# Performance work log

Measured on AMD Instinct MI355X. Metric: run time of the kernel, lower is better.

## Reference

```python
import jax, jax.numpy as jnp
import numpy as np

B, IN, OUT, E, K = 8192, 512, 720, 16, 2
MOE_TEMP = 1.0


def setup_inputs() -> dict:
    key = jax.random.key(0)
    ks = jax.random.split(key, 5)
    s_in = 1.0 / np.sqrt(IN)
    return {
        "x": jax.random.normal(ks[0], (B, IN), dtype=jnp.float32),
        "Wg": jax.random.normal(ks[1], (IN, E), dtype=jnp.float32) * s_in,
        "bg": jax.random.normal(ks[2], (E,), dtype=jnp.float32) * 0.01,
        "We": jax.random.normal(ks[3], (E, IN, OUT), dtype=jnp.float32) * s_in,
        "be": jax.random.normal(ks[4], (E, OUT), dtype=jnp.float32) * 0.01,
    }


def reference(x, Wg, bg, We, be):
    # Gating (eval mode: no noise, divide by temperature)
    gate = (x @ Wg + bg) / MOE_TEMP                      # [B, E]
    topk_vals, topk_idx = jax.lax.top_k(gate, K)          # [B, K]
    gates = jax.nn.softmax(topk_vals, axis=1)             # [B, K]

    # Dense all-expert forward (as the original module computes)
    expert_out = jnp.einsum('bi,eio->beo', x, We) + be    # [B, E, OUT]
    sel = jnp.take_along_axis(expert_out, topk_idx[:, :, None], axis=1)  # [B, K, OUT]
    output = jnp.sum(gates[:, :, None] * sel, axis=1)     # [B, OUT]

    # Load-balancing loss
    probs = jax.nn.softmax(gate, axis=1)                  # [B, E]
    assign = jnp.argmax(gate, axis=1)                     # [B]
    D = jnp.zeros((E,), dtype=gate.dtype).at[assign].add(1.0) / x.shape[0]
    P = jnp.mean(probs, axis=0)
    lb_loss = jnp.sum(D * P) * E
    return output, lb_loss
```

## Files before the change

kernel.cpp:

```cpp
#include <hip/hip_runtime.h>
#include <hip/hip_bf16.h>


#define BATCH 8192
#define IND   512
#define OUTD  720
#define NEXP  16
#define NGBLK 512

typedef __attribute__((ext_vector_type(8))) short short8;
typedef __attribute__((ext_vector_type(4))) float floatx4;

__device__ __forceinline__ unsigned short f2bf(float f) {
    union { float f; unsigned u; } v; v.f = f;
    unsigned r = v.u + 0x7FFFu + ((v.u >> 16) & 1u);
    return (unsigned short)(r >> 16);
}
__device__ __forceinline__ float bf2f(unsigned short u) {
    union { unsigned u; float f; } v; v.u = ((unsigned)u) << 16;
    return v.f;
}

__device__ __forceinline__ void gl2lds16(const void* g, void* l) {
    __builtin_amdgcn_global_load_lds(
        (const __attribute__((address_space(1))) void*)g,
        (__attribute__((address_space(3))) void*)l, 16, 0, 0);
}

__global__ __launch_bounds__(256) void prep_kernel(
    const float* __restrict__ x, const float* __restrict__ Wg,
    const float* __restrict__ bg, const float* __restrict__ We,
    float* __restrict__ gates, int* __restrict__ rowinfo,
    unsigned char* __restrict__ cnt8, float* __restrict__ Pblk, float* __restrict__ Dblk,
    unsigned short* __restrict__ xb, unsigned short* __restrict__ Wt)
{
    __shared__ __align__(16) char smem[35328];
    int tid = threadIdx.x;

    if (blockIdx.x < NGBLK) {
        float* sWg   = (float*)smem;
        float* sg    = sWg + 16 * 516;
        float* smax  = sg + 16 * 17;
        float* sinv  = smax + 16;
        int*   sasgn = (int*)(sinv + 16);

        int rbase = blockIdx.x * 16;

        const float4* gw4 = (const float4*)Wg;
        #pragma unroll
        for (int j = 0; j < 8; ++j) {
            int f = tid + j * 256;
            float4 v = gw4[f];
            int i  = f >> 2;
            int e0 = (f & 3) * 4;
            sWg[(e0 + 0) * 516 + i] = v.x;
            sWg[(e0 + 1) * 516 + i] = v.y;
            sWg[(e0 + 2) * 516 + i] = v.z;
            sWg[(e0 + 3) * 516 + i] = v.w;
        }

        const float4* gx4 = (const float4*)(x + (size_t)rbase * IND);
        #pragma unroll
        for (int j = 0; j < 4; ++j) {
            int f = tid + j * 256;
            float4 v0 = gx4[2 * f];
            float4 v1 = gx4[2 * f + 1];
            short8 o;
            o[0] = (short)f2bf(v0.x); o[1] = (short)f2bf(v0.y);
            o[2] = (short)f2bf(v0.z); o[3] = (short)f2bf(v0.w);
            o[4] = (short)f2bf(v1.x); o[5] = (short)f2bf(v1.y);
            o[6] = (short)f2bf(v1.z); o[7] = (short)f2bf(v1.w);
            *(short8*)&xb[(size_t)rbase * IND + (size_t)f * 8] = o;
        }
        __syncthreads();

        int r = tid >> 4, e = tid & 15;
        const float4* xr = (const float4*)(x + (size_t)(rbase + r) * IND);
        const float4* wr = (const float4*)&sWg[e * 516];
        float acc = bg[e];
        #pragma unroll 8
        for (int i4 = 0; i4 < 128; ++i4) {
            float4 a = xr[i4], w = wr[i4];
            acc += a.x * w.x + a.y * w.y + a.z * w.z + a.w * w.w;
        }
        sg[r * 17 + e] = acc;
        __syncthreads();

        if (tid < 16) {
            int row = rbase + tid;
            float v0 = -1e30f, v1 = -1e30f; int i0 = 0, i1 = 0;
            float g[16];
            #pragma unroll
            for (int ee = 0; ee < 16; ++ee) {
                float v = sg[tid * 17 + ee]; g[ee] = v;
                if (v > v0)      { v1 = v0; i1 = i0; v0 = v; i0 = ee; }
                else if (v > v1) { v1 = v;  i1 = ee; }
            }
            float e1   = expf(v1 - v0);
            float inv2 = 1.f / (1.f + e1);
            gates[row * 2 + 0] = inv2;
            gates[row * 2 + 1] = e1 * inv2;

            float ssum = 0.f;
            #pragma unroll
            for (int ee = 0; ee < 16; ++ee) ssum += expf(g[ee] - v0);
            smax[tid]  = v0;
            sinv[tid]  = 1.f / ssum;
            sasgn[tid] = i0 | (i1 << 8);
        }
        __syncthreads();

        if (tid < 16) {
            int me  = sasgn[tid];
            int i0  = me & 255, i1 = me >> 8;
            int p0 = 0, p1 = 0;
            for (int rp = 0; rp < tid; ++rp) {
                int a = sasgn[rp];
                int a0 = a & 255, a1 = a >> 8;
                p0 += (a0 == i0) + (a1 == i0);
                p1 += (a0 == i1) + (a1 == i1);
            }
            rowinfo[rbase + tid] = i0 | (i1 << 4) | (p0 << 8) | (p1 << 13);

            int ee = tid;
            int cnt = 0; float D = 0.f, P = 0.f;
            #pragma unroll
            for (int rp = 0; rp < 16; ++rp) {
                int a = sasgn[rp];
                int a0 = a & 255, a1 = a >> 8;
                cnt += (a0 == ee) + (a1 == ee);
                D   += (a0 == ee) ? 1.f : 0.f;
                P   += expf(sg[rp * 17 + ee] - smax[rp]) * sinv[rp];
            }
            cnt8[blockIdx.x * 16 + ee] = (unsigned char)cnt;
            Dblk[blockIdx.x * 16 + ee] = D;
            Pblk[blockIdx.x * 16 + ee] = P;
        }
    } else {
        float* tile = (float*)smem;
        int t  = blockIdx.x - NGBLK;
        int e  = t / 184;
        int rem = t - e * 184;
        int kb = (rem / 23) * 64;
        int ob = (rem % 23) * 32;
        const float* src = We + (size_t)e * (IND * OUTD);

        #pragma unroll
        for (int p = 0; p < 2; ++p) {
            int f  = tid + p * 256;
            int kk = f >> 3;
            int o4 = f & 7;
            float4 v = make_float4(0.f, 0.f, 0.f, 0.f);
            if (ob + o4 * 4 < OUTD)
                v = *(const float4*)&src[(size_t)(kb + kk) * OUTD + ob + o4 * 4];
            tile[(o4 * 4 + 0) * 69 + kk] = v.x;
            tile[(o4 * 4 + 1) * 69 + kk] = v.y;
            tile[(o4 * 4 + 2) * 69 + kk] = v.z;
            tile[(o4 * 4 + 3) * 69 + kk] = v.w;
        }
        __syncthreads();

        int o  = tid >> 3;
        int k8 = tid & 7;
        if (ob + o < OUTD) {
            const float* sp = &tile[o * 69 + k8 * 8];
            short8 wv;
            #pragma unroll
            for (int q = 0; q < 8; ++q) wv[q] = (short)f2bf(sp[q]);
            *(short8*)&Wt[(size_t)e * (OUTD * IND) + (size_t)(ob + o) * IND + kb + k8 * 8] = wv;
        }
    }
}

__global__ __launch_bounds__(256, 4) void moe_mfma_kernel(
    const unsigned short* __restrict__ xb, const unsigned short* __restrict__ Wt,
    const float* __restrict__ be,
    const unsigned char* __restrict__ cnt8, const int* __restrict__ rowinfo,
    const float* __restrict__ gates,
    unsigned short* __restrict__ partial)
{
    int e = blockIdx.z;
    int r0 = blockIdx.y * 128;
    int n0 = blockIdx.x * 96;

    __shared__ unsigned short sAB[14336];
    __shared__ unsigned short sbase[513];
    __shared__ int   schunk[16];
    __shared__ int   srow[128];
    __shared__ float sgw[128];
    __shared__ unsigned short sent[128];

    int tid = threadIdx.x;

    sbase[tid]       = cnt8[tid * 16 + e];
    sbase[tid + 256] = cnt8[(tid + 256) * 16 + e];
    __syncthreads();
    if (tid < 16) {
        int s = 0;
        #pragma unroll
        for (int j = 0; j < 32; ++j) s += sbase[tid * 32 + j];
        schunk[tid] = s;
    }
    __syncthreads();
    if (tid == 0) {
        int run = 0;
        #pragma unroll
        for (int c = 0; c < 16; ++c) { int s = schunk[c]; schunk[c] = run; run += s; }
        sbase[512] = (unsigned short)run;
    }
    __syncthreads();
    if (tid < 16) {
        int run = schunk[tid];
        #pragma unroll
        for (int j = 0; j < 32; ++j) {
            int c = sbase[tid * 32 + j];
            sbase[tid * 32 + j] = (unsigned short)run;
            run += c;
        }
    }
    __syncthreads();
    int n = sbase[512];
    if (r0 >= n) return;

    if (tid < 128) {
        int idx = r0 + tid;
        if (idx < n) {
            int g = 0;
            #pragma unroll
            for (int step = 256; step; step >>= 1)
                if (g + step <= 511 && (int)sbase[g + step] <= idx) g += step;
            int local = idx - (int)sbase[g];
            int row = 0, k = 0;
            #pragma unroll
            for (int r = 0; r < 16; ++r) {
                int info = rowinfo[g * 16 + r];
                int i0 = info & 15, i1 = (info >> 4) & 15;
                int p0 = (info >> 8) & 31, p1 = (info >> 13) & 31;
                if (i0 == e && p0 == local) { row = g * 16 + r; k = 0; }
                if (i1 == e && p1 == local) { row = g * 16 + r; k = 1; }
            }
            srow[tid] = row;
            sgw[tid]  = gates[row * 2 + k];
            sent[tid] = (unsigned short)((row << 1) | k);
        } else { srow[tid] = 0; sgw[tid] = 0.f; sent[tid] = 0; }
    }
    __syncthreads();

    int lane = tid & 63, wave = tid >> 6;
    int lsub = lane >> 3;
    int swz  = (lane & 7) ^ lsub;

    const unsigned short* aglb[4];
    unsigned short* alds[4];
    #pragma unroll
    for (int g = 0; g < 4; ++g) {
        int row = wave * 32 + g * 8 + lsub;
        aglb[g] = xb + (size_t)srow[row] * IND + swz * 8;
        alds[g] = &sAB[(wave * 32 + g * 8) * 64];
    }
    const unsigned short* bglb[3];
    unsigned short* blds[3];
    #pragma unroll
    for (int g = 0; g < 3; ++g) {
        int col = n0 + wave * 24 + g * 8 + lsub;
        if (col >= OUTD) col = 0;
        bglb[g] = Wt + ((size_t)e * OUTD + col) * IND + swz * 8;
        blds[g] = &sAB[8192 + (wave * 24 + g * 8) * 64];
    }

    int l15 = lane & 15, quad = lane >> 4;
    int wm = (wave & 1) * 64, wn = (wave >> 1) * 48;
    int axor = (l15 & 7) * 8;

    floatx4 acc[4][3] = {};

    for (int kt = 0; kt < IND / 64; ++kt) {
        __syncthreads();
        #pragma unroll
        for (int g = 0; g < 4; ++g) gl2lds16(aglb[g] + kt * 64, alds[g]);
        #pragma unroll
        for (int g = 0; g < 3; ++g) gl2lds16(bglb[g] + kt * 64, blds[g]);
        __syncthreads();

        #pragma unroll
        for (int ks = 0; ks < 2; ++ks) {
            int ko = ((ks * 4 + quad) * 8) ^ axor;
            short8 a[4], b[3];
            #pragma unroll
            for (int i = 0; i < 4; ++i) a[i] = *(const short8*)&sAB[(wm + i * 16 + l15) * 64 + ko];
            #pragma unroll
            for (int j = 0; j < 3; ++j) b[j] = *(const short8*)&sAB[8192 + (wn + j * 16 + l15) * 64 + ko];
            #pragma unroll
            for (int i = 0; i < 4; ++i)
                #pragma unroll
                for (int j = 0; j < 3; ++j)
                    acc[i][j] = __builtin_amdgcn_mfma_f32_16x16x32_bf16(a[i], b[j], acc[i][j], 0, 0, 0);
        }
    }

    __syncthreads();
    #pragma unroll
    for (int j = 0; j < 3; ++j) {
        int coll = wn + j * 16 + l15;
        int gcol = n0 + coll;
        float bev = (gcol < OUTD) ? be[e * OUTD + gcol] : 0.f;
        #pragma unroll
        for (int i = 0; i < 4; ++i) {
            #pragma unroll
            for (int rr = 0; rr < 4; ++rr) {
                int rowl = wm + i * 16 + quad * 4 + rr;
                sAB[rowl * 104 + coll] = f2bf(sgw[rowl] * (acc[i][j][rr] + bev));
            }
        }
    }
    __syncthreads();

    #pragma unroll
    for (int p = 0; p < 6; ++p) {
        int c    = tid + p * 256;
        int rowl = c / 12;
        int ch   = c - rowl * 12;
        int gcol = n0 + ch * 8;
        if (gcol < OUTD && r0 + rowl < n) {
            *(short8*)&partial[(size_t)sent[rowl] * OUTD + gcol] =
                *(const short8*)&sAB[rowl * 104 + ch * 8];
        }
    }
}

__global__ __launch_bounds__(256) void combine_kernel(
    const unsigned short* __restrict__ partial,
    const float* __restrict__ Pblk, const float* __restrict__ Dblk,
    float* __restrict__ out)
{
    __shared__ float sredP[256], sredD[256];
    unsigned f = blockIdx.x * 256 + threadIdx.x;
    unsigned b = f / 180u;
    unsigned o4 = (f - b * 180u) * 4u;
    const unsigned short* p0 = partial + (size_t)(2u * b) * OUTD + o4;
    ushort4 u0 = *(const ushort4*)p0;
    ushort4 u1 = *(const ushort4*)(p0 + OUTD);
    float4 rv;
    rv.x = bf2f(u0.x) + bf2f(u1.x);
    rv.y = bf2f(u0.y) + bf2f(u1.y);
    rv.z = bf2f(u0.z) + bf2f(u1.z);
    rv.w = bf2f(u0.w) + bf2f(u1.w);
    *(float4*)(out + (size_t)b * OUTD + o4) = rv;

    if (blockIdx.x == 0) {
        int tid = threadIdx.x;
        int e = tid & 15, stripe = tid >> 4;
        float accP = 0.f, accD = 0.f;
        for (int j = 0; j < 32; ++j) {
            int g = stripe * 32 + j;
            accP += Pblk[g * 16 + e];
            accD += Dblk[g * 16 + e];
        }
        sredP[tid] = accP; sredD[tid] = accD;
        __syncthreads();
        if (tid == 0) {
            float s = 0.f;
            for (int ee = 0; ee < 16; ++ee) {
                float P = 0.f, D = 0.f;
                #pragma unroll
                for (int st = 0; st < 16; ++st) { P += sredP[st * 16 + ee]; D += sredD[st * 16 + ee]; }
                s += (D / (float)BATCH) * (P / (float)BATCH);
            }
            out[(size_t)BATCH * OUTD] = s * (float)NEXP;
        }
    }
}

extern "C" void kernel_launch(void* const* d_in, const int* in_sizes, int n_in,
                              void* d_out, int out_size, void* d_ws, size_t ws_size,
                              hipStream_t stream)
{
    const float* x  = (const float*)d_in[0];
    const float* Wg = (const float*)d_in[1];
    const float* bg = (const float*)d_in[2];
    const float* We = (const float*)d_in[3];
    const float* be = (const float*)d_in[4];
    float* out = (float*)d_out;

    char* ws = (char*)d_ws;
    float* gates   = (float*)ws;
    int*   rowinfo = (int*)(ws + 65536);
    unsigned char* cnt8 = (unsigned char*)(ws + 98304);
    float* Pblk    = (float*)(ws + 106496);
    float* Dblk    = (float*)(ws + 139264);
    size_t off_xb  = 172032;
    unsigned short* xb = (unsigned short*)(ws + off_xb);
    size_t off_wt = off_xb + (size_t)BATCH * IND * 2;
    unsigned short* Wt = (unsigned short*)(ws + off_wt);
    size_t off_pt = off_wt + (size_t)NEXP * OUTD * IND * 2;
    unsigned short* partial = (unsigned short*)(ws + off_pt);

    prep_kernel<<<NGBLK + 2944, 256, 0, stream>>>(x, Wg, bg, We, gates, rowinfo,
                                                  cnt8, Pblk, Dblk, xb, Wt);

    dim3 grid(8, 10, NEXP);
    moe_mfma_kernel<<<grid, 256, 0, stream>>>(xb, Wt, be, cnt8, rowinfo, gates, partial);

    combine_kernel<<<(BATCH * (OUTD / 4)) / 256, 256, 0, stream>>>(partial, Pblk, Dblk, out);
}
```

Measured before the change: 140.7 us.

## Drop LDS staging of gate weights and double transpose tile depth in prep kernel

The gating blocks no longer stage Wg into shared memory. Each thread now reads Wg straight from global memory, where it is cached because every block reads the same data. This shrinks the shared-memory allocation, removes a barrier, and allows a launch bound of 8 blocks per CU. The weight-transpose blocks now handle 128 k-rows per tile instead of 64, halving the transpose block count and giving each thread two bf16 vector stores. The trade-off is strided, uncoalesced scalar global loads of Wg in the gating dot product, plus larger per-block transpose work.

```diff
diff --git a/kernel.cpp b/kernel.cpp
--- a/kernel.cpp
+++ b/kernel.cpp
@@ -27,37 +27,23 @@
         (__attribute__((address_space(3))) void*)l, 16, 0, 0);
 }
 
-__global__ __launch_bounds__(256) void prep_kernel(
+__global__ __launch_bounds__(256, 8) void prep_kernel(
     const float* __restrict__ x, const float* __restrict__ Wg,
     const float* __restrict__ bg, const float* __restrict__ We,
     float* __restrict__ gates, int* __restrict__ rowinfo,
     unsigned char* __restrict__ cnt8, float* __restrict__ Pblk, float* __restrict__ Dblk,
     unsigned short* __restrict__ xb, unsigned short* __restrict__ Wt)
 {
-    __shared__ __align__(16) char smem[35328];
+    __shared__ __align__(16) char smem[16896];
     int tid = threadIdx.x;
 
     if (blockIdx.x < NGBLK) {
-        float* sWg   = (float*)smem;
-        float* sg    = sWg + 16 * 516;
+        float* sg    = (float*)smem;
         float* smax  = sg + 16 * 17;
         float* sinv  = smax + 16;
         int*   sasgn = (int*)(sinv + 16);
 
         int rbase = blockIdx.x * 16;
-
-        const float4* gw4 = (const float4*)Wg;
-        #pragma unroll
-        for (int j = 0; j < 8; ++j) {
-            int f = tid + j * 256;
-            float4 v = gw4[f];
-            int i  = f >> 2;
-            int e0 = (f & 3) * 4;
-            sWg[(e0 + 0) * 516 + i] = v.x;
-            sWg[(e0 + 1) * 516 + i] = v.y;
-            sWg[(e0 + 2) * 516 + i] = v.z;
-            sWg[(e0 + 3) * 516 + i] = v.w;
-        }
 
         const float4* gx4 = (const float4*)(x + (size_t)rbase * IND);
         #pragma unroll
@@ -72,16 +58,16 @@
             o[6] = (short)f2bf(v1.z); o[7] = (short)f2bf(v1.w);
             *(short8*)&xb[(size_t)rbase * IND + (size_t)f * 8] = o;
         }
-        __syncthreads();
 
         int r = tid >> 4, e = tid & 15;
-        const float4* xr = (const float4*)(x + (size_t)(rbase + r) * IND);
-        const float4* wr = (const float4*)&sWg[e * 516];
+        const float*  xrp = x + (size_t)(rbase + r) * IND;
+        const float*  wgp = Wg + e;
         float acc = bg[e];
-        #pragma unroll 8
-        for (int i4 = 0; i4 < 128; ++i4) {
-            float4 a = xr[i4], w = wr[i4];
-            acc += a.x * w.x + a.y * w.y + a.z * w.z + a.w * w.w;
+        #pragma unroll 4
+        for (int i = 0; i < IND; i += 4) {
+            float4 xa = *(const float4*)(xrp + i);
+            acc += xa.x * wgp[(i + 0) * 16] + xa.y * wgp[(i + 1) * 16]
+                 + xa.z * wgp[(i + 2) * 16] + xa.w * wgp[(i + 3) * 16];
         }
         sg[r * 17 + e] = acc;
         __syncthreads();
@@ -139,35 +125,40 @@
     } else {
         float* tile = (float*)smem;
         int t  = blockIdx.x - NGBLK;
-        int e  = t / 184;
-        int rem = t - e * 184;
-        int kb = (rem / 23) * 64;
+        int e  = t / 92;
+        int rem = t - e * 92;
+        int kb = (rem / 23) * 128;
         int ob = (rem % 23) * 32;
         const float* src = We + (size_t)e * (IND * OUTD);
 
         #pragma unroll
-        for (int p = 0; p < 2; ++p) {
+        for (int p = 0; p < 4; ++p) {
             int f  = tid + p * 256;
             int kk = f >> 3;
             int o4 = f & 7;
             float4 v = make_float4(0.f, 0.f, 0.f, 0.f);
             if (ob + o4 * 4 < OUTD)
                 v = *(const float4*)&src[(size_t)(kb + kk) * OUTD + ob + o4 * 4];
-            tile[(o4 * 4 + 0) * 69 + kk] = v.x;
-            tile[(o4 * 4 + 1) * 69 + kk] = v.y;
-            tile[(o4 * 4 + 2) * 69 + kk] = v.z;
-            tile[(o4 * 4 + 3) * 69 + kk] = v.w;
+            tile[(o4 * 4 + 0) * 132 + kk] = v.x;
+            tile[(o4 * 4 + 1) * 132 + kk] = v.y;
+            tile[(o4 * 4 + 2) * 132 + kk] = v.z;
+            tile[(o4 * 4 + 3) * 132 + kk] = v.w;
         }
         __syncthreads();
 
         int o  = tid >> 3;
         int k8 = tid & 7;
         if (ob + o < OUTD) {
-            const float* sp = &tile[o * 69 + k8 * 8];
-            short8 wv;
-            #pragma unroll
-            for (int q = 0; q < 8; ++q) wv[q] = (short)f2bf(sp[q]);
-            *(short8*)&Wt[(size_t)e * (OUTD * IND) + (size_t)(ob + o) * IND + kb + k8 * 8] = wv;
+            unsigned short* dst = Wt + (size_t)e * (OUTD * IND) + (size_t)(ob + o) * IND + kb;
+            #pragma unroll
+            for (int h = 0; h < 2; ++h) {
+                int kc = h * 8 + k8;
+                const float* sp = &tile[o * 132 + kc * 8];
+                short8 wv;
+                #pragma unroll
+                for (int q = 0; q < 8; ++q) wv[q] = (short)f2bf(sp[q]);
+                *(short8*)&dst[kc * 8] = wv;
+            }
         }
     }
 }
@@ -395,7 +386,7 @@
     size_t off_pt = off_wt + (size_t)NEXP * OUTD * IND * 2;
     unsigned short* partial = (unsigned short*)(ws + off_pt);
 
-    prep_kernel<<<NGBLK + 2944, 256, 0, stream>>>(x, Wg, bg, We, gates, rowinfo,
+    prep_kernel<<<NGBLK + 1472, 256, 0, stream>>>(x, Wg, bg, We, gates, rowinfo,
                                                   cnt8, Pblk, Dblk, xb, Wt);
 
     dim3 grid(8, 10, NEXP);
```

After: 150.9 us. 7.3% more time.
